# Optimization experiments

Hardware: AMD Instinct MI355X
Metric: run time of the kernel (lower is better)

## Reference

```python
import jax, jax.numpy as jnp
import numpy as np

N = 300000        # occupied voxels
G = 128           # voxel grid side
C_IN = 128
C_OUT = 32
TIMES = C_IN // C_OUT
K = 27            # 3^3 kernel offsets


def _build_kernel_map():
    """Sample N unique voxels in a G^3 grid and build the 27-offset neighbor map.
    nbr[k, n] = index of the voxel at coords[n] + offset[k], or N if absent."""
    rng = np.random.default_rng(0)
    lin = rng.choice(G ** 3, size=N, replace=False).astype(np.int64)
    coords = np.stack(np.unravel_index(lin, (G, G, G)), axis=1).astype(np.int64)  # [N,3]
    lookup = np.full(G ** 3, N, dtype=np.int32)
    lookup[lin] = np.arange(N, dtype=np.int32)
    offs = np.stack(np.meshgrid(*[[-1, 0, 1]] * 3, indexing='ij'), axis=-1).reshape(-1, 3)  # [27,3]
    nbr = np.empty((K, N), dtype=np.int32)
    for k, off in enumerate(offs):
        nc = coords + off
        valid = np.all((nc >= 0) & (nc < G), axis=1)
        li = (nc[:, 0] * G + nc[:, 1]) * G + nc[:, 2]
        nbr[k] = np.where(valid, lookup[np.clip(li, 0, G ** 3 - 1)], N)
    return nbr


def setup_inputs() -> dict:
    key = jax.random.key(0)
    k1, k2, k3, k4 = jax.random.split(key, 4)
    feats = jax.random.normal(k1, (N, C_IN), dtype=jnp.float32)
    W0 = jax.random.normal(k2, (K, C_IN, C_IN), dtype=jnp.float32) * 0.05
    W1 = jax.random.normal(k3, (K, C_IN, C_OUT), dtype=jnp.float32) * 0.05
    W2 = jax.random.normal(k4, (K, C_OUT, C_OUT), dtype=jnp.float32) * 0.05
    nbr_idx = jnp.asarray(_build_kernel_map())
    return {"feats": feats, "W0": W0, "W1": W1, "W2": W2, "nbr_idx": nbr_idx}


def sparse_conv(x, W, nbr):
    """Gather-GEMM-accumulate sparse conv: out[n] = sum_k x[nbr[k,n]] @ W[k].
    Missing neighbors (index N) gather a zero row."""
    xp = jnp.concatenate([x, jnp.zeros((1, x.shape[1]), x.dtype)], axis=0)  # [N+1,Cin]
    out0 = jnp.zeros((x.shape[0], W.shape[2]), x.dtype)

    def body(acc, kw):
        idx, Wk = kw
        return acc + xp[idx] @ Wk, None

    out, _ = jax.lax.scan(body, out0, (nbr, W))
    return out


def reference(feats, W0, W1, W2, nbr_idx):
    n = feats.shape[0]
    # mean over channel groups: [N, times, C_out] -> [N, C_out]
    downsampled = jnp.mean(feats.reshape(n, TIMES, C_OUT), axis=1)
    upsampled = jnp.tile(downsampled, (1, TIMES))           # [N, C_in]
    residual = feats - upsampled
    residual = sparse_conv(residual, W0, nbr_idx)           # C_in -> C_in
    residual = sparse_conv(residual, W1, nbr_idx)           # C_in -> C_out
    residual = sparse_conv(residual, W2, nbr_idx)           # C_out -> C_out
    return downsampled + residual
```

## Files before the change

kernel.cpp:

```cpp
#include <hip/hip_runtime.h>

#define DEVINL __device__ __forceinline__

typedef __attribute__((ext_vector_type(8))) __bf16 bf16x8;
typedef __attribute__((ext_vector_type(4))) float f32x4;
typedef __attribute__((ext_vector_type(8))) unsigned short u16x8;

DEVINL unsigned short f2bf(float x) {
  unsigned u = __builtin_bit_cast(unsigned, x);
  u += 0x7FFFu + ((u >> 16) & 1u);
  return (unsigned short)(u >> 16);
}

#define BARRIER() asm volatile("s_barrier" ::: "memory")

template <int N>
DEVINL void waitvm() {
  asm volatile("s_waitcnt vmcnt(%0)" ::"n"(N) : "memory");
}

DEVINL void gload16(const void* g, void* l) {
  __builtin_amdgcn_global_load_lds(
      (const __attribute__((address_space(1))) void*)g,
      (__attribute__((address_space(3))) void*)l, 16, 0, 0);
}

__global__ __launch_bounds__(256) void prep_kernel(
    const float* __restrict__ F, unsigned short* __restrict__ RES,
    float* __restrict__ DS, int n) {
  const int t = threadIdx.x;
  const int row = blockIdx.x * 16 + (t >> 4);
  const int cg = t & 15;
  if (row >= n) return;
  const float4* f4 = (const float4*)(F + (size_t)row * 128 + cg * 8);
  float4 v0 = f4[0], v1 = f4[1];
  float v[8] = {v0.x, v0.y, v0.z, v0.w, v1.x, v1.y, v1.z, v1.w};
  float s[8] = {v0.x, v0.y, v0.z, v0.w, v1.x, v1.y, v1.z, v1.w};
#pragma unroll
  for (int i = 0; i < 8; ++i) s[i] += __shfl_xor(s[i], 4);
#pragma unroll
  for (int i = 0; i < 8; ++i) s[i] += __shfl_xor(s[i], 8);
  u16x8 rb;
#pragma unroll
  for (int i = 0; i < 8; ++i) rb[i] = f2bf(v[i] - 0.25f * s[i]);
  *(u16x8*)(RES + (size_t)row * 128 + cg * 8) = rb;
  if (cg < 4) {
    float4 d0 = {0.25f * s[0], 0.25f * s[1], 0.25f * s[2], 0.25f * s[3]};
    float4 d1 = {0.25f * s[4], 0.25f * s[5], 0.25f * s[6], 0.25f * s[7]};
    float4* dp = (float4*)(DS + (size_t)row * 32 + cg * 8);
    dp[0] = d0;
    dp[1] = d1;
  }
}

template <int CIN, int COUT>
DEVINL void pack_one(const float* __restrict__ W, unsigned short* __restrict__ P, int g) {
  const int n = g % COUT;
  const int t = g / COUT;
  const int q = t & 3;
  const int t2 = t >> 2;
  const int ks = t2 % (CIN / 32);
  const int k = t2 / (CIN / 32);
  const float* src = W + ((size_t)k * CIN + ks * 32 + q * 8) * COUT + n;
  unsigned short* dst = P + (size_t)g * 8;
#pragma unroll
  for (int j = 0; j < 8; ++j) dst[j] = f2bf(src[(size_t)j * COUT]);
}

__global__ __launch_bounds__(256) void pack_kernel(
    const float* __restrict__ W0, const float* __restrict__ W1,
    const float* __restrict__ W2, unsigned short* __restrict__ P0,
    unsigned short* __restrict__ P1, unsigned short* __restrict__ P2) {
  int g = blockIdx.x * 256 + threadIdx.x;
  if (g < 55296)
    pack_one<128, 128>(W0, P0, g);
  else if (g < 69120)
    pack_one<128, 32>(W1, P1, g - 55296);
  else if (g < 72576)
    pack_one<32, 32>(W2, P2, g - 69120);
}

__global__ void zero_tail(unsigned short* a, unsigned short* b, unsigned short* c) {
  int t = threadIdx.x;
  if (t < 128) { a[t] = 0; b[t] = 0; }
  if (t < 32) c[t] = 0;
}

template <int CIN, int COUT, int WM, int WN, bool FINAL, int MINB>
__global__ __launch_bounds__(256, MINB) void spconv(
    const unsigned short* __restrict__ X, const unsigned short* __restrict__ Bp,
    const int* __restrict__ nbr, unsigned short* __restrict__ Y,
    float* __restrict__ OUT, const float* __restrict__ DS, int nr) {
  constexpr int BM = 128;
  constexpr int KS = CIN / 32;
  constexpr int WROWS = BM / WM;
  constexpr int WCOLS = COUT / WN;
  constexpr int MF = WROWS / 16;
  constexpr int NF = WCOLS / 16;
  constexpr int CPR = CIN / 8;
  constexpr int SWZ = (CPR < 8 ? CPR - 1 : 7);
  constexpr int ROWB = CIN * 2;
  constexpr int ACH = BM * CPR;
  constexpr int APF = ACH / 256;
  constexpr int NB = KS * NF;

  __shared__ unsigned short As[2][BM * CIN];
  __shared__ int IdxS[27 * BM];

  const int tid = threadIdx.x;
  const int lane = tid & 63;
  const int wave = tid >> 6;
  const int wm = wave / WN;
  const int wn = wave % WN;
  const int base = blockIdx.x * BM;
  const int q = lane >> 4;
  const int l16 = lane & 15;

  for (int f = tid; f < 27 * BM; f += 256) {
    int nn = base + (f & (BM - 1));
    IdxS[f] = (nn < nr) ? nbr[(size_t)(f >> 7) * nr + nn] : nr;
  }
  __syncthreads();

  const unsigned short* bbase = Bp + ((size_t)q * COUT + wn * WCOLS + l16) * 8;

  bf16x8 bA[NB], bB[NB];

  auto loadB = [&](bf16x8(&dst)[NB], int k) {
#pragma unroll
    for (int ks = 0; ks < KS; ++ks)
#pragma unroll
      for (int j = 0; j < NF; ++j)
        dst[ks * NF + j] = *(const bf16x8*)(
            bbase + ((size_t)k * CIN * COUT) + ((size_t)(ks * 4) * COUT + j * 16) * 8);
  };

  auto issueA = [&](int k) {
    const int kb = k & 1;
#pragma unroll
    for (int pp = 0; pp < APF; ++pp) {
      int slot = pp * 256 + tid;
      int r = slot / CPR;
      int cc = (slot % CPR) * 16;
      int c = (cc ^ ((r & SWZ) << 4)) >> 4;
      int g = IdxS[k * BM + r];
      gload16(X + (size_t)g * CIN + c * 8, (char*)(&As[kb][0]) + slot * 16);
    }
  };

  f32x4 acc[MF][NF] = {};

  auto mfmaStep = [&](int kb, const bf16x8(&bf)[NB]) {
    const char* Ab = (const char*)(&As[kb][0]);
#pragma unroll
    for (int ks = 0; ks < KS; ++ks) {
      bf16x8 af[MF];
#pragma unroll
      for (int i = 0; i < MF; ++i) {
        int r = wm * WROWS + i * 16 + l16;
        int db = r * ROWB + (((ks * 64 + q * 16) & (ROWB - 1)) ^ ((r & SWZ) << 4));
        af[i] = __builtin_bit_cast(bf16x8, *(const uint4*)(Ab + db));
      }
#pragma unroll
      for (int i = 0; i < MF; ++i)
#pragma unroll
        for (int j = 0; j < NF; ++j)
          acc[i][j] = __builtin_amdgcn_mfma_f32_16x16x32_bf16(af[i], bf[ks * NF + j],
                                                              acc[i][j], 0, 0, 0);
    }
  };

  loadB(bA, 0);
  issueA(0);

#pragma unroll 1
  for (int k = 0; k < 26; k += 2) {
    loadB(bB, k + 1);
    issueA(k + 1);
    waitvm<NB + APF>();
    BARRIER();
    mfmaStep(0, bA);
    BARRIER();
    if (k + 2 < 27) {
      loadB(bA, k + 2);
      issueA(k + 2);
      waitvm<NB + APF>();
    } else {
      waitvm<0>();
    }
    BARRIER();
    mfmaStep(1, bB);
    BARRIER();
  }
  waitvm<0>();
  BARRIER();
  mfmaStep(0, bA);

#pragma unroll
  for (int i = 0; i < MF; ++i)
#pragma unroll
    for (int j = 0; j < NF; ++j)
#pragma unroll
      for (int r = 0; r < 4; ++r) {
        int row = base + wm * WROWS + i * 16 + q * 4 + r;
        int col = wn * WCOLS + j * 16 + l16;
        if (row < nr) {
          float v = acc[i][j][r];
          if constexpr (FINAL)
            OUT[(size_t)row * COUT + col] = v + DS[(size_t)row * COUT + col];
          else
            Y[(size_t)row * COUT + col] = f2bf(v);
        }
      }
}

extern "C" void kernel_launch(void* const* d_in, const int* in_sizes, int n_in,
                              void* d_out, int out_size, void* d_ws, size_t ws_size,
                              hipStream_t stream) {
  const float* feats = (const float*)d_in[0];
  const float* W0 = (const float*)d_in[1];
  const float* W1 = (const float*)d_in[2];
  const float* W2 = (const float*)d_in[3];
  const int* nbr = (const int*)d_in[4];
  const int n = in_sizes[0] / 128;
  float* out = (float*)d_out;

  char* p = (char*)d_ws;
  auto take = [&](size_t bytes) {
    char* r = p;
    p += (bytes + 255) & ~(size_t)255;
    return r;
  };
  unsigned short* resB = (unsigned short*)take((size_t)(n + 1) * 128 * 2);
  unsigned short* y0 = (unsigned short*)take((size_t)(n + 1) * 128 * 2);
  unsigned short* y1 = (unsigned short*)take((size_t)(n + 1) * 32 * 2);
  float* ds = (float*)take((size_t)n * 32 * 4);
  unsigned short* p0 = (unsigned short*)take((size_t)27 * 128 * 128 * 2);
  unsigned short* p1 = (unsigned short*)take((size_t)27 * 128 * 32 * 2);
  unsigned short* p2 = (unsigned short*)take((size_t)27 * 32 * 32 * 2);

  prep_kernel<<<(n + 15) / 16, 256, 0, stream>>>(feats, resB, ds, n);
  pack_kernel<<<284, 256, 0, stream>>>(W0, W1, W2, p0, p1, p2);
  zero_tail<<<1, 128, 0, stream>>>(resB + (size_t)n * 128, y0 + (size_t)n * 128,
                                   y1 + (size_t)n * 32);
  const int gb = (n + 127) / 128;
  spconv<128, 128, 1, 4, false, 2>
      <<<gb, 256, 0, stream>>>(resB, p0, nbr, y0, nullptr, nullptr, n);
  spconv<128, 32, 4, 1, false, 2>
      <<<gb, 256, 0, stream>>>(y0, p1, nbr, y1, nullptr, nullptr, n);
  spconv<32, 32, 4, 1, true, 4>
      <<<gb, 256, 0, stream>>>(y1, p2, nbr, nullptr, out, ds, n);
}
```

Measured before the change: 551.4 us.

## Compact valid neighbors per offset in first sparse conv to skip empty rows

Replaces the first 128->128 sparse conv with a kernel that, per offset, ballot-scans which rows of a 256-row block have a valid neighbor and compacts them into 32-row tiles. Only those tiles are gathered and multiplied, and results are scattered into an fp32 LDS accumulator with atomics before a final bf16 write. With sparse occupancy (~14% density), most neighbor slots are empty, so this avoids MFMA work and gathers of zero rows. In exchange it adds LDS atomics, extra barriers, a large LDS footprint limiting occupancy to one block per CU, and serialized scan steps.

```diff
diff --git a/kernel.cpp b/kernel.cpp
--- a/kernel.cpp
+++ b/kernel.cpp
@@ -84,6 +84,160 @@
   int t = threadIdx.x;
   if (t < 128) { a[t] = 0; b[t] = 0; }
   if (t < 32) c[t] = 0;
+}
+
+__global__ __launch_bounds__(512, 1) void spconv_sp(
+    const unsigned short* __restrict__ X, const unsigned short* __restrict__ Bp,
+    const int* __restrict__ nbr, unsigned short* __restrict__ Y, int nr) {
+  constexpr int CIN = 128, COUT = 128;
+  constexpr int BM = 256, MT = 32;
+  constexpr int KS = CIN / 32;
+  constexpr int NF = 2;
+  constexpr int NB = KS * NF;
+  constexpr int ACCW = COUT + 4;
+
+  __shared__ float accS[BM * ACCW];
+  __shared__ unsigned short As[2][MT * CIN];
+  __shared__ int klist[3][BM];
+  __shared__ int meta[3];
+  __shared__ int wsum[8];
+
+  const int tid = threadIdx.x;
+  const int lane = tid & 63;
+  const int wave = tid >> 6;
+  const int q = lane >> 4;
+  const int l16 = lane & 15;
+  const int wm = wave >> 2;
+  const int wn = wave & 3;
+  const int base = blockIdx.x * BM;
+
+  const unsigned short* bbase = Bp + ((size_t)q * COUT + wn * 32 + l16) * 8;
+
+  bf16x8 bf0[NB], bf1[NB];
+
+  auto loadB = [&](bf16x8(&dst)[NB], int k) {
+#pragma unroll
+    for (int ks = 0; ks < KS; ++ks)
+#pragma unroll
+      for (int j = 0; j < NF; ++j)
+        dst[ks * NF + j] = *(const bf16x8*)(
+            bbase + (size_t)k * CIN * COUT + ((size_t)(ks * 4) * COUT + j * 16) * 8);
+  };
+
+  auto issueA = [&](int kb, int tt, int bufsel) {
+    int r = tid >> 4;
+    int cc = (tid & 15) << 4;
+    int c = (cc ^ ((r & 7) << 4)) >> 4;
+    int g = klist[kb][tt * MT + r] & 0x7FFFF;
+    gload16(X + (size_t)g * CIN + c * 8, (char*)(&As[bufsel][0]) + tid * 16);
+  };
+
+  auto scanPublish = [&](int k, int v) {
+    bool valid = (tid < BM) && (base + tid < nr) && (v != nr);
+    unsigned long long b = __ballot(valid);
+    if (lane == 0) wsum[wave] = __popcll(b);
+    int lanePre = __popcll(b & ((1ull << lane) - 1));
+    __syncthreads();
+    int pre = lanePre, cnt = 0;
+#pragma unroll
+    for (int w = 0; w < 4; ++w) {
+      int c = wsum[w];
+      if (w < wave) pre += c;
+      cnt += c;
+    }
+    int kb = k % 3;
+    if (valid) klist[kb][pre] = v | (tid << 19);
+    int padded = ((cnt + MT - 1) / MT) * MT;
+    if (padded == 0) padded = MT;
+    if (tid < padded - cnt) klist[kb][cnt + tid] = nr;
+    if (tid == 0) meta[kb] = padded / MT;
+    __syncthreads();
+  };
+
+  auto tileCompute = [&](int bufsel, const bf16x8(&bf)[NB], int kb, int tt) {
+    const char* Ab = (const char*)(&As[bufsel][0]);
+    f32x4 tc[NF] = {};
+    const int r = wm * 16 + l16;
+#pragma unroll
+    for (int ks = 0; ks < KS; ++ks) {
+      bf16x8 af = __builtin_bit_cast(
+          bf16x8,
+          *(const uint4*)(Ab + r * 256 + (((ks * 64 + q * 16) & 255) ^ ((r & 7) << 4))));
+#pragma unroll
+      for (int j = 0; j < NF; ++j)
+        tc[j] = __builtin_amdgcn_mfma_f32_16x16x32_bf16(af, bf[ks * NF + j], tc[j], 0, 0, 0);
+    }
+#pragma unroll
+    for (int rr = 0; rr < 4; ++rr) {
+      int o = klist[kb][tt * MT + wm * 16 + q * 4 + rr] >> 19;
+      float* ap = &accS[o * ACCW + wn * 32 + l16];
+#pragma unroll
+      for (int j = 0; j < NF; ++j) atomicAdd(ap + j * 16, tc[j][rr]);
+    }
+  };
+
+  for (int i = tid; i < BM * ACCW; i += 512) accS[i] = 0.f;
+  {
+    int v0 = nr;
+    if (tid < BM && base + tid < nr) v0 = nbr[base + tid];
+    scanPublish(0, v0);
+    int v1 = nr;
+    if (tid < BM && base + tid < nr) v1 = nbr[(size_t)nr + base + tid];
+    scanPublish(1, v1);
+  }
+  int vPre = nr;
+  if (tid < BM && base + tid < nr) vPre = nbr[(size_t)2 * nr + base + tid];
+
+  loadB(bf0, 0);
+  issueA(0, 0, 0);
+  int bp = 0;
+
+#pragma unroll 1
+  for (int k = 0; k < 27; ++k) {
+    const int kb = k % 3;
+    const int T = meta[kb];
+#pragma unroll 1
+    for (int tt = 0; tt < T; ++tt) {
+      const bool lastT = (tt == T - 1);
+      if (!lastT) {
+        issueA(kb, tt + 1, bp ^ 1);
+        waitvm<1>();
+      } else if (k < 26) {
+        issueA((k + 1) % 3, 0, bp ^ 1);
+        if (k & 1) loadB(bf0, k + 1);
+        else loadB(bf1, k + 1);
+        waitvm<NB + 1>();
+      } else {
+        waitvm<0>();
+      }
+      BARRIER();
+      if (k & 1) tileCompute(bp, bf1, kb, tt);
+      else tileCompute(bp, bf0, kb, tt);
+      if (tt == 0 && k + 2 < 27) {
+        scanPublish(k + 2, vPre);
+        if (k + 3 < 27) {
+          vPre = nr;
+          if (tid < BM && base + tid < nr)
+            vPre = nbr[(size_t)(k + 3) * nr + base + tid];
+        }
+      }
+      BARRIER();
+      bp ^= 1;
+    }
+  }
+
+  __syncthreads();
+  for (int s = tid; s < BM * (COUT / 8); s += 512) {
+    int rrow = s >> 4, c8 = (s & 15) << 3;
+    int row = base + rrow;
+    if (row < nr) {
+      const float* ap = &accS[rrow * ACCW + c8];
+      u16x8 ob;
+#pragma unroll
+      for (int i = 0; i < 8; ++i) ob[i] = f2bf(ap[i]);
+      *(u16x8*)(Y + (size_t)row * COUT + c8) = ob;
+    }
+  }
 }
 
 template <int CIN, int COUT, int WM, int WN, bool FINAL, int MINB>
@@ -243,9 +397,9 @@
   pack_kernel<<<284, 256, 0, stream>>>(W0, W1, W2, p0, p1, p2);
   zero_tail<<<1, 128, 0, stream>>>(resB + (size_t)n * 128, y0 + (size_t)n * 128,
                                    y1 + (size_t)n * 32);
+  const int gb0 = (n + 255) / 256;
+  spconv_sp<<<gb0, 512, 0, stream>>>(resB, p0, nbr, y0, n);
   const int gb = (n + 127) / 128;
-  spconv<128, 128, 1, 4, false, 2>
-      <<<gb, 256, 0, stream>>>(resB, p0, nbr, y0, nullptr, nullptr, n);
   spconv<128, 32, 4, 1, false, 2>
       <<<gb, 256, 0, stream>>>(y0, p1, nbr, y1, nullptr, nullptr, n);
   spconv<32, 32, 4, 1, true, 4>
```

New measurement: 2.020 ms. 3.66x slower.
